# Kernel tuning notes

Hardware: AMD Instinct MI355X
Metric: run time of the kernel (lower is better)

The kernel has to match this reference:

```python
import jax, jax.numpy as jnp
import numpy as np

TEMPERATURE = 0.5
B, D = 4096, 256


def setup_inputs() -> dict:
    key = jax.random.key(0)
    k1, k2 = jax.random.split(key)
    emb_i = jax.random.normal(k1, (B, D), dtype=jnp.float32)
    emb_j = jax.random.normal(k2, (B, D), dtype=jnp.float32)
    return {"emb_i": emb_i, "emb_j": emb_j}


def reference(emb_i, emb_j):
    # NT-Xent (SimCLR) loss, vectorized version of the per-sample python loop.
    n = emb_i.shape[0]
    eps = 1e-12
    z_i = emb_i / jnp.maximum(jnp.linalg.norm(emb_i, axis=1, keepdims=True), eps)
    z_j = emb_j / jnp.maximum(jnp.linalg.norm(emb_j, axis=1, keepdims=True), eps)
    reps = jnp.concatenate([z_i, z_j], axis=0)               # [2N, D], unit rows
    # cosine similarity of unit vectors == dot product
    sim = reps @ reps.T                                       # [2N, 2N]
    exp_sim = jnp.exp(sim / TEMPERATURE)
    # denominator for row i: sum over k != i of exp(sim[i,k]/T)
    denom = jnp.sum(exp_sim, axis=1) - jnp.diagonal(exp_sim)  # [2N]
    # positive-pair sims: sim[k, k+N] and sim[k+N, k]
    pos = jnp.concatenate([jnp.diagonal(sim[:n, n:]), jnp.diagonal(sim[n:, :n])])
    # l_ij = log(exp(pos/T) / denom) = pos/T - log(denom)
    loss_terms = pos / TEMPERATURE - jnp.log(denom)
    return (1.0 / (2 * n)) * jnp.sum(loss_terms)
```

## Files before the change

### kernel.cpp

```cpp
#include <hip/hip_runtime.h>
#include <math.h>


#define NROWS 8192
#define NHALF 4096
#define DIM   256
#define BM    128
#define BN    128
#define BK    64
#define NCB   (NROWS / BN)
#define NTRI  (NCB * (NCB + 1) / 2)

typedef __attribute__((ext_vector_type(8))) short bf16x8;
typedef __attribute__((ext_vector_type(4))) float f32x4;

static __device__ __forceinline__ unsigned short f2bf(float x) {
  unsigned int u = __float_as_uint(x);
  unsigned int r = (u + 0x7FFFu + ((u >> 16) & 1u)) >> 16;
  return (unsigned short)r;
}

__global__ __launch_bounds__(256) void normalize_kernel(
    const float* __restrict__ emb_i, const float* __restrict__ emb_j,
    unsigned short* __restrict__ zb, float* __restrict__ out) {
  if (blockIdx.x == 0 && threadIdx.x == 0) out[0] = 0.f;
  int w = threadIdx.x >> 6, lane = threadIdx.x & 63;
  int row = blockIdx.x * 4 + w;
  const float* src = (row < NHALF) ? (emb_i + (size_t)row * DIM)
                                   : (emb_j + (size_t)(row - NHALF) * DIM);
  float4 v = ((const float4*)src)[lane];
  float ss = v.x * v.x + v.y * v.y + v.z * v.z + v.w * v.w;
  #pragma unroll
  for (int off = 32; off; off >>= 1) ss += __shfl_down(ss, off, 64);
  float total = __shfl(ss, 0, 64);
  float inv = 1.0f / fmaxf(sqrtf(total), 1e-12f);
  ushort4 o;
  o.x = f2bf(v.x * inv); o.y = f2bf(v.y * inv);
  o.z = f2bf(v.z * inv); o.w = f2bf(v.w * inv);
  ((ushort4*)&zb[(size_t)row * DIM])[lane] = o;
}

__global__ __launch_bounds__(256) void denom_kernel(
    const unsigned short* __restrict__ zb, float* __restrict__ denomP,
    float* __restrict__ posv) {
  __shared__ unsigned short As[BM * BK];
  __shared__ unsigned short Bs[BN * BK];

  int t = blockIdx.x;
  int by = (int)((sqrtf(8.0f * (float)t + 1.0f) - 1.0f) * 0.5f);
  while ((by + 1) * (by + 2) / 2 <= t) ++by;
  while (by * (by + 1) / 2 > t) --by;
  int bx = t - by * (by + 1) / 2;

  const int tid = threadIdx.x;
  const int w = tid >> 6;
  const int lane = tid & 63;
  const int wr = w >> 1, wc = w & 1;
  const int quad = lane >> 4;
  const int m16 = lane & 15;
  const int row0 = bx * BM;
  const int col0 = by * BN;

  f32x4 acc[4][4];
  #pragma unroll
  for (int i = 0; i < 4; ++i)
    #pragma unroll
    for (int j = 0; j < 4; ++j) {
      f32x4 z4 = {0.f, 0.f, 0.f, 0.f};
      acc[i][j] = z4;
    }

  for (int kc = 0; kc < DIM; kc += BK) {
    #pragma unroll
    for (int tt = 0; tt < 4; ++tt) {
      int rbase = w * 32 + tt * 8;
      int gr = rbase + (lane >> 3);
      int gk = kc + (lane & 7) * 8;
      __builtin_amdgcn_global_load_lds(
          (const __attribute__((address_space(1))) unsigned int*)
              &zb[(size_t)(row0 + gr) * DIM + gk],
          (__attribute__((address_space(3))) unsigned int*)&As[rbase * BK],
          16, 0, 0);
      __builtin_amdgcn_global_load_lds(
          (const __attribute__((address_space(1))) unsigned int*)
              &zb[(size_t)(col0 + gr) * DIM + gk],
          (__attribute__((address_space(3))) unsigned int*)&Bs[rbase * BK],
          16, 0, 0);
    }
    __syncthreads();

    #pragma unroll
    for (int ks = 0; ks < BK; ks += 32) {
      bf16x8 af[4], bfr[4];
      #pragma unroll
      for (int i = 0; i < 4; ++i)
        af[i] = *(const bf16x8*)&As[(wr * 64 + i * 16 + m16) * BK + ks + quad * 8];
      #pragma unroll
      for (int j = 0; j < 4; ++j)
        bfr[j] = *(const bf16x8*)&Bs[(wc * 64 + j * 16 + m16) * BK + ks + quad * 8];
      #pragma unroll
      for (int i = 0; i < 4; ++i)
        #pragma unroll
        for (int j = 0; j < 4; ++j)
          acc[i][j] = __builtin_amdgcn_mfma_f32_16x16x32_bf16(
              af[i], bfr[j], acc[i][j], 0, 0, 0);
    }
    __syncthreads();
  }

  if (col0 - row0 == NHALF) {
    #pragma unroll
    for (int i = 0; i < 4; ++i)
      #pragma unroll
      for (int j = 0; j < 4; ++j) {
        int gcol = col0 + wc * 64 + j * 16 + m16;
        #pragma unroll
        for (int r = 0; r < 4; ++r) {
          int grow = row0 + wr * 64 + i * 16 + quad * 4 + r;
          if (gcol - grow == NHALF) posv[grow] = acc[i][j][r];
        }
      }
  }

  float rs[4][4];
  float cs[4] = {0.f, 0.f, 0.f, 0.f};
  #pragma unroll
  for (int i = 0; i < 4; ++i)
    #pragma unroll
    for (int r = 0; r < 4; ++r) rs[i][r] = 0.f;

  #pragma unroll
  for (int i = 0; i < 4; ++i)
    #pragma unroll
    for (int j = 0; j < 4; ++j) {
      int gcol = col0 + wc * 64 + j * 16 + m16;
      #pragma unroll
      for (int r = 0; r < 4; ++r) {
        int grow = row0 + wr * 64 + i * 16 + quad * 4 + r;
        float e = (grow == gcol) ? 0.f : __expf(2.0f * acc[i][j][r]);
        rs[i][r] += e;
        cs[j] += e;
      }
    }

  float* red = (float*)As;

  #pragma unroll
  for (int i = 0; i < 4; ++i)
    #pragma unroll
    for (int r = 0; r < 4; ++r) {
      float v = rs[i][r];
      v += __shfl_xor(v, 1, 16);
      v += __shfl_xor(v, 2, 16);
      v += __shfl_xor(v, 4, 16);
      v += __shfl_xor(v, 8, 16);
      if (m16 == 0) red[wc * 128 + wr * 64 + i * 16 + quad * 4 + r] = v;
    }
  #pragma unroll
  for (int j = 0; j < 4; ++j) {
    float v = cs[j];
    v += __shfl_xor(v, 16, 64);
    v += __shfl_xor(v, 32, 64);
    if (quad == 0) red[256 + wr * 128 + wc * 64 + j * 16 + m16] = v;
  }
  __syncthreads();

  if (tid < 128) {
    denomP[(size_t)by * NROWS + row0 + tid] = red[tid] + red[128 + tid];
  } else if (bx != by) {
    int c = tid - 128;
    denomP[(size_t)bx * NROWS + col0 + c] = red[256 + c] + red[384 + c];
  }
}

__global__ __launch_bounds__(256) void reduce_kernel(
    const float* __restrict__ denomP, const float* __restrict__ posv,
    float* __restrict__ out) {
  int tid = threadIdx.x;
  int r = blockIdx.x * 256 + tid;
  float s = 0.f;
  #pragma unroll 8
  for (int b = 0; b < NCB; ++b) s += denomP[(size_t)b * NROWS + r];
  float v = -logf(s);
  if (r < NHALF) v += 4.0f * posv[r];
  #pragma unroll
  for (int off = 32; off; off >>= 1) v += __shfl_down(v, off, 64);
  __shared__ float s4[4];
  if ((tid & 63) == 0) s4[tid >> 6] = v;
  __syncthreads();
  if (tid == 0)
    atomicAdd(out, (s4[0] + s4[1] + s4[2] + s4[3]) * (1.0f / 8192.0f));
}

extern "C" void kernel_launch(void* const* d_in, const int* in_sizes, int n_in,
                              void* d_out, int out_size, void* d_ws,
                              size_t ws_size, hipStream_t stream) {
  const float* emb_i = (const float*)d_in[0];
  const float* emb_j = (const float*)d_in[1];
  unsigned short* zb = (unsigned short*)d_ws;
  float* denomP = (float*)(zb + (size_t)NROWS * DIM);
  float* posv = denomP + (size_t)NCB * NROWS;
  float* out = (float*)d_out;

  normalize_kernel<<<NROWS / 4, 256, 0, stream>>>(emb_i, emb_j, zb, out);
  denom_kernel<<<NTRI, 256, 0, stream>>>(zb, denomP, posv);
  reduce_kernel<<<NROWS / 256, 256, 0, stream>>>(denomP, posv, out);
}
```

Baseline: 111.7 us.

## Double-buffer LDS tiles and XOR-swizzle layout in the similarity GEMM

The denom kernel's K loop now uses two LDS buffers per operand. It issues the global-to-LDS load for the next K chunk before running the MFMAs on the current one, so memory latency can overlap with compute and one barrier per step is removed. The 16-byte chunks within each LDS row are also XOR-swizzled by row index, which is meant to cut bank conflicts on the bf16x8 fragment reads. The cost is double the LDS use per block (64 KB), which may limit occupancy, and slightly more address arithmetic.

```diff
diff --git a/kernel.cpp b/kernel.cpp
--- a/kernel.cpp
+++ b/kernel.cpp
@@ -43,8 +43,8 @@
 __global__ __launch_bounds__(256) void denom_kernel(
     const unsigned short* __restrict__ zb, float* __restrict__ denomP,
     float* __restrict__ posv) {
-  __shared__ unsigned short As[BM * BK];
-  __shared__ unsigned short Bs[BN * BK];
+  __shared__ unsigned short As[2][BM * BK];
+  __shared__ unsigned short Bs[2][BN * BK];
 
   int t = blockIdx.x;
   int by = (int)((sqrtf(8.0f * (float)t + 1.0f) - 1.0f) * 0.5f);
@@ -61,6 +61,10 @@
   const int row0 = bx * BM;
   const int col0 = by * BN;
 
+  const unsigned short* zbA = zb + (size_t)row0 * DIM;
+  const unsigned short* zbB = zb + (size_t)col0 * DIM;
+  const int swz = ((lane & 7) ^ (lane >> 3)) * 8;
+
   f32x4 acc[4][4];
   #pragma unroll
   for (int i = 0; i < 4; ++i)
@@ -70,34 +74,41 @@
       acc[i][j] = z4;
     }
 
-  for (int kc = 0; kc < DIM; kc += BK) {
+  auto stage = [&](int b, int kc) {
     #pragma unroll
     for (int tt = 0; tt < 4; ++tt) {
       int rbase = w * 32 + tt * 8;
       int gr = rbase + (lane >> 3);
-      int gk = kc + (lane & 7) * 8;
+      int gk = kc + swz;
       __builtin_amdgcn_global_load_lds(
           (const __attribute__((address_space(1))) unsigned int*)
-              &zb[(size_t)(row0 + gr) * DIM + gk],
-          (__attribute__((address_space(3))) unsigned int*)&As[rbase * BK],
+              &zbA[(size_t)gr * DIM + gk],
+          (__attribute__((address_space(3))) unsigned int*)&As[b][rbase * BK],
           16, 0, 0);
       __builtin_amdgcn_global_load_lds(
           (const __attribute__((address_space(1))) unsigned int*)
-              &zb[(size_t)(col0 + gr) * DIM + gk],
-          (__attribute__((address_space(3))) unsigned int*)&Bs[rbase * BK],
+              &zbB[(size_t)gr * DIM + gk],
+          (__attribute__((address_space(3))) unsigned int*)&Bs[b][rbase * BK],
           16, 0, 0);
     }
-    __syncthreads();
-
+  };
+
+  auto compute = [&](int b) {
     #pragma unroll
     for (int ks = 0; ks < BK; ks += 32) {
       bf16x8 af[4], bfr[4];
       #pragma unroll
-      for (int i = 0; i < 4; ++i)
-        af[i] = *(const bf16x8*)&As[(wr * 64 + i * 16 + m16) * BK + ks + quad * 8];
-      #pragma unroll
-      for (int j = 0; j < 4; ++j)
-        bfr[j] = *(const bf16x8*)&Bs[(wc * 64 + j * 16 + m16) * BK + ks + quad * 8];
+      for (int i = 0; i < 4; ++i) {
+        int row = wr * 64 + i * 16 + m16;
+        af[i] = *(const bf16x8*)
+            &As[b][row * BK + ((((ks >> 3) + quad) ^ (m16 & 7)) * 8)];
+      }
+      #pragma unroll
+      for (int j = 0; j < 4; ++j) {
+        int row = wc * 64 + j * 16 + m16;
+        bfr[j] = *(const bf16x8*)
+            &Bs[b][row * BK + ((((ks >> 3) + quad) ^ (m16 & 7)) * 8)];
+      }
       #pragma unroll
       for (int i = 0; i < 4; ++i)
         #pragma unroll
@@ -105,8 +116,18 @@
           acc[i][j] = __builtin_amdgcn_mfma_f32_16x16x32_bf16(
               af[i], bfr[j], acc[i][j], 0, 0, 0);
     }
+  };
+
+  stage(0, 0);
+  __syncthreads();
+  #pragma unroll
+  for (int kc = BK; kc < DIM; kc += BK) {
+    const int nb = (kc >> 6) & 1;
+    stage(nb, kc);
+    compute(nb ^ 1);
     __syncthreads();
   }
+  compute(1);
 
   if (col0 - row0 == NHALF) {
     #pragma unroll
```

Result: faster. 106.9 us (-4.3%).

## Pre-swizzle normalized embeddings into MFMA fragment layout and load operands directly from global

Applied to the files above, without the earlier changes.

The normalize kernel now writes bf16 rows in a fragment-ordered layout (16-row groups, per k-step blocks), so the Gram kernel can load MFMA operands straight from global memory into registers with double-buffered prefetch, dropping LDS staging and barriers. The sqrt(2) scale is folded into the normalization so exp no longer needs a multiply by 2, and off-diagonal tiles skip the diagonal mask. In exchange, operands are fetched from global/L2 per wave with no LDS sharing between waves, and bf16 rounding now happens on sqrt(2)-scaled values.

```diff
diff --git a/kernel.cpp b/kernel.cpp
--- a/kernel.cpp
+++ b/kernel.cpp
@@ -7,7 +7,6 @@
 #define DIM   256
 #define BM    128
 #define BN    128
-#define BK    64
 #define NCB   (NROWS / BN)
 #define NTRI  (NCB * (NCB + 1) / 2)
 
@@ -22,29 +21,40 @@
 
 __global__ __launch_bounds__(256) void normalize_kernel(
     const float* __restrict__ emb_i, const float* __restrict__ emb_j,
-    unsigned short* __restrict__ zb, float* __restrict__ out) {
+    unsigned short* __restrict__ zbF, float* __restrict__ out) {
+  __shared__ unsigned short tile[16 * DIM];
   if (blockIdx.x == 0 && threadIdx.x == 0) out[0] = 0.f;
-  int w = threadIdx.x >> 6, lane = threadIdx.x & 63;
-  int row = blockIdx.x * 4 + w;
-  const float* src = (row < NHALF) ? (emb_i + (size_t)row * DIM)
-                                   : (emb_j + (size_t)(row - NHALF) * DIM);
-  float4 v = ((const float4*)src)[lane];
-  float ss = v.x * v.x + v.y * v.y + v.z * v.z + v.w * v.w;
-  #pragma unroll
-  for (int off = 32; off; off >>= 1) ss += __shfl_down(ss, off, 64);
-  float total = __shfl(ss, 0, 64);
-  float inv = 1.0f / fmaxf(sqrtf(total), 1e-12f);
-  ushort4 o;
-  o.x = f2bf(v.x * inv); o.y = f2bf(v.y * inv);
-  o.z = f2bf(v.z * inv); o.w = f2bf(v.w * inv);
-  ((ushort4*)&zb[(size_t)row * DIM])[lane] = o;
-}
-
-__global__ __launch_bounds__(256) void denom_kernel(
-    const unsigned short* __restrict__ zb, float* __restrict__ denomP,
+  const int w = threadIdx.x >> 6, lane = threadIdx.x & 63;
+  const int rg = blockIdx.x;
+  #pragma unroll
+  for (int rr = 0; rr < 4; ++rr) {
+    const int m16 = w * 4 + rr;
+    const int row = rg * 16 + m16;
+    const float* src = (row < NHALF) ? (emb_i + (size_t)row * DIM)
+                                     : (emb_j + (size_t)(row - NHALF) * DIM);
+    float4 v = ((const float4*)src)[lane];
+    float ss = v.x * v.x + v.y * v.y + v.z * v.z + v.w * v.w;
+    #pragma unroll
+    for (int off = 32; off; off >>= 1) ss += __shfl_down(ss, off, 64);
+    float total = __shfl(ss, 0, 64);
+    float inv = 1.41421356237f / fmaxf(sqrtf(total), 1e-12f);
+    ushort4 o;
+    o.x = f2bf(v.x * inv); o.y = f2bf(v.y * inv);
+    o.z = f2bf(v.z * inv); o.w = f2bf(v.w * inv);
+    const int ks = lane >> 3, quad = (lane >> 1) & 3, jj = (lane & 1) * 4;
+    *(ushort4*)&tile[ks * 512 + (quad * 16 + m16) * 8 + jj] = o;
+  }
+  __syncthreads();
+  uint4* dst = (uint4*)(zbF + (size_t)rg * (16 * DIM));
+  const uint4* srcT = (const uint4*)tile;
+  dst[threadIdx.x] = srcT[threadIdx.x];
+  dst[256 + threadIdx.x] = srcT[256 + threadIdx.x];
+}
+
+__global__ __launch_bounds__(256, 3) void denom_kernel(
+    const unsigned short* __restrict__ zbF, float* __restrict__ denomP,
     float* __restrict__ posv) {
-  __shared__ unsigned short As[BM * BK];
-  __shared__ unsigned short Bs[BN * BK];
+  __shared__ float red[512];
 
   int t = blockIdx.x;
   int by = (int)((sqrtf(8.0f * (float)t + 1.0f) - 1.0f) * 0.5f);
@@ -61,6 +71,14 @@
   const int row0 = bx * BM;
   const int col0 = by * BN;
 
+  const unsigned short* pA[4];
+  const unsigned short* pB[4];
+  #pragma unroll
+  for (int i = 0; i < 4; ++i) {
+    pA[i] = zbF + (size_t)(bx * 8 + wr * 4 + i) * 4096 + lane * 8;
+    pB[i] = zbF + (size_t)(by * 8 + wc * 4 + i) * 4096 + lane * 8;
+  }
+
   f32x4 acc[4][4];
   #pragma unroll
   for (int i = 0; i < 4; ++i)
@@ -70,43 +88,34 @@
       acc[i][j] = z4;
     }
 
-  for (int kc = 0; kc < DIM; kc += BK) {
-    #pragma unroll
-    for (int tt = 0; tt < 4; ++tt) {
-      int rbase = w * 32 + tt * 8;
-      int gr = rbase + (lane >> 3);
-      int gk = kc + (lane & 7) * 8;
-      __builtin_amdgcn_global_load_lds(
-          (const __attribute__((address_space(1))) unsigned int*)
-              &zb[(size_t)(row0 + gr) * DIM + gk],
-          (__attribute__((address_space(3))) unsigned int*)&As[rbase * BK],
-          16, 0, 0);
-      __builtin_amdgcn_global_load_lds(
-          (const __attribute__((address_space(1))) unsigned int*)
-              &zb[(size_t)(col0 + gr) * DIM + gk],
-          (__attribute__((address_space(3))) unsigned int*)&Bs[rbase * BK],
-          16, 0, 0);
-    }
-    __syncthreads();
-
-    #pragma unroll
-    for (int ks = 0; ks < BK; ks += 32) {
-      bf16x8 af[4], bfr[4];
-      #pragma unroll
-      for (int i = 0; i < 4; ++i)
-        af[i] = *(const bf16x8*)&As[(wr * 64 + i * 16 + m16) * BK + ks + quad * 8];
-      #pragma unroll
-      for (int j = 0; j < 4; ++j)
-        bfr[j] = *(const bf16x8*)&Bs[(wc * 64 + j * 16 + m16) * BK + ks + quad * 8];
-      #pragma unroll
-      for (int i = 0; i < 4; ++i)
-        #pragma unroll
-        for (int j = 0; j < 4; ++j)
-          acc[i][j] = __builtin_amdgcn_mfma_f32_16x16x32_bf16(
-              af[i], bfr[j], acc[i][j], 0, 0, 0);
-    }
-    __syncthreads();
-  }
+#define LOADAB(A, B, ks)                                          \
+  do {                                                            \
+    _Pragma("unroll") for (int i = 0; i < 4; ++i) {               \
+      A[i] = *(const bf16x8*)(pA[i] + (ks) * 512);                \
+      B[i] = *(const bf16x8*)(pB[i] + (ks) * 512);                \
+    }                                                             \
+  } while (0)
+
+#define MFMA16(A, B)                                              \
+  do {                                                            \
+    _Pragma("unroll") for (int i = 0; i < 4; ++i)                 \
+        _Pragma("unroll") for (int j = 0; j < 4; ++j)             \
+            acc[i][j] = __builtin_amdgcn_mfma_f32_16x16x32_bf16(  \
+                A[i], B[j], acc[i][j], 0, 0, 0);                  \
+  } while (0)
+
+  bf16x8 aE[4], bE[4], aO[4], bO[4];
+  LOADAB(aE, bE, 0);
+  LOADAB(aO, bO, 1);
+  #pragma unroll
+  for (int k2 = 0; k2 < 4; ++k2) {
+    MFMA16(aE, bE);
+    if (k2 < 3) LOADAB(aE, bE, 2 * k2 + 2);
+    MFMA16(aO, bO);
+    if (k2 < 3) LOADAB(aO, bO, 2 * k2 + 3);
+  }
+#undef LOADAB
+#undef MFMA16
 
   if (col0 - row0 == NHALF) {
     #pragma unroll
@@ -129,21 +138,32 @@
     #pragma unroll
     for (int r = 0; r < 4; ++r) rs[i][r] = 0.f;
 
-  #pragma unroll
-  for (int i = 0; i < 4; ++i)
-    #pragma unroll
-    for (int j = 0; j < 4; ++j) {
-      int gcol = col0 + wc * 64 + j * 16 + m16;
+  if (bx != by) {
+    #pragma unroll
+    for (int i = 0; i < 4; ++i)
       #pragma unroll
-      for (int r = 0; r < 4; ++r) {
-        int grow = row0 + wr * 64 + i * 16 + quad * 4 + r;
-        float e = (grow == gcol) ? 0.f : __expf(2.0f * acc[i][j][r]);
-        rs[i][r] += e;
-        cs[j] += e;
+      for (int j = 0; j < 4; ++j)
+        #pragma unroll
+        for (int r = 0; r < 4; ++r) {
+          float e = __expf(acc[i][j][r]);
+          rs[i][r] += e;
+          cs[j] += e;
+        }
+  } else {
+    #pragma unroll
+    for (int i = 0; i < 4; ++i)
+      #pragma unroll
+      for (int j = 0; j < 4; ++j) {
+        int gcol = col0 + wc * 64 + j * 16 + m16;
+        #pragma unroll
+        for (int r = 0; r < 4; ++r) {
+          int grow = row0 + wr * 64 + i * 16 + quad * 4 + r;
+          float e = (grow == gcol) ? 0.f : __expf(acc[i][j][r]);
+          rs[i][r] += e;
+          cs[j] += e;
+        }
       }
-    }
-
-  float* red = (float*)As;
+  }
 
   #pragma unroll
   for (int i = 0; i < 4; ++i)
@@ -182,7 +202,7 @@
   #pragma unroll 8
   for (int b = 0; b < NCB; ++b) s += denomP[(size_t)b * NROWS + r];
   float v = -logf(s);
-  if (r < NHALF) v += 4.0f * posv[r];
+  if (r < NHALF) v += 2.0f * posv[r];
   #pragma unroll
   for (int off = 32; off; off >>= 1) v += __shfl_down(v, off, 64);
   __shared__ float s4[4];
@@ -197,12 +217,12 @@
                               size_t ws_size, hipStream_t stream) {
   const float* emb_i = (const float*)d_in[0];
   const float* emb_j = (const float*)d_in[1];
-  unsigned short* zb = (unsigned short*)d_ws;
-  float* denomP = (float*)(zb + (size_t)NROWS * DIM);
+  unsigned short* zbF = (unsigned short*)d_ws;
+  float* denomP = (float*)(zbF + (size_t)NROWS * DIM);
   float* posv = denomP + (size_t)NCB * NROWS;
   float* out = (float*)d_out;
 
-  normalize_kernel<<<NROWS / 4, 256, 0, stream>>>(emb_i, emb_j, zb, out);
-  denom_kernel<<<NTRI, 256, 0, stream>>>(zb, denomP, posv);
+  normalize_kernel<<<NROWS / 16, 256, 0, stream>>>(emb_i, emb_j, zbF, out);
+  denom_kernel<<<NTRI, 256, 0, stream>>>(zbF, denomP, posv);
   reduce_kernel<<<NROWS / 256, 256, 0, stream>>>(denomP, posv, out);
 }
```

After: 99.85 us. 10.6% less time.
